# Kernel tuning notes

Measured on AMD Instinct MI355X. Metric: run time of the kernel, lower is better.

## Reference

```python
import jax, jax.numpy as jnp
import numpy as np

N = 100000      # node_size
R = 2000        # rel_size
E = 300000      # triple_size == nnz(adj)
ER = 300000     # nnz of node-to-rel adjacency
EE = 300000     # nnz of node-to-node adjacency
NODE_F = 128
REL_F = 128
ENT_F = NODE_F + REL_F  # 256
DEPTH = 2


def setup_inputs() -> dict:
    key = jax.random.key(0)
    ks = jax.random.split(key, 14)
    return {
        'ent_emb': jax.random.normal(ks[0], (N, NODE_F), jnp.float32) * 0.1,
        'rel_emb': jax.random.normal(ks[1], (R, REL_F), jnp.float32) * 0.1,
        'a_self': jax.random.normal(ks[2], (ENT_F, 1), jnp.float32) * 0.1,
        'a_neigh': jax.random.normal(ks[3], (ENT_F, 1), jnp.float32) * 0.1,
        'a_rel': jax.random.normal(ks[4], (REL_F, 1), jnp.float32) * 0.1,
        'sp_val': jax.random.uniform(ks[5], (E,), jnp.float32),
        'adj_row': jax.random.randint(ks[6], (E,), 0, N),
        'adj_col': jax.random.randint(ks[7], (E,), 0, N),
        'sp_row': jnp.arange(E),
        'sp_col': jax.random.randint(ks[8], (E,), 0, R),
        'rel_row': jax.random.randint(ks[9], (ER,), 0, N),
        'rel_col': jax.random.randint(ks[10], (ER,), 0, R),
        'ent_row': jax.random.randint(ks[11], (EE,), 0, N),
        'ent_col': jax.random.randint(ks[12], (EE,), 0, N),
    }


def _mean_agg(row, col, emb, nrows):
    # tf.sparse_softmax over all-ones values == 1/deg per row -> row mean
    deg = jax.ops.segment_sum(jnp.ones(row.shape, emb.dtype), row, nrows)
    w = 1.0 / deg[row]
    return jax.ops.segment_sum(w[:, None] * emb[col], row, nrows)


def _segment_softmax(vals, seg, nseg):
    m = jax.ops.segment_max(vals, seg, nseg)
    e = jnp.exp(vals - m[seg])
    s = jax.ops.segment_sum(e, seg, nseg)
    return e / s[seg]


def reference(ent_emb, rel_emb, a_self, a_neigh, a_rel, sp_val,
              adj_row, adj_col, sp_row, sp_col, rel_row, rel_col, ent_row, ent_col):
    # initial features: mean-aggregated entity + relation features
    rel_feat = _mean_agg(rel_row, rel_col, rel_emb, N)
    ent_feat = _mean_agg(ent_row, ent_col, ent_emb, N)
    features = jax.nn.relu(jnp.concatenate([ent_feat, rel_feat], axis=-1))  # [N, ENT_F]
    outputs = [features]

    # per-edge relation attention term: (T,R) sparse @ (rel_emb @ a_rel); constant across depth
    rel_proj = (rel_emb @ a_rel)[:, 0]                               # [R]
    rel_attn = jax.ops.segment_sum(sp_val * rel_proj[sp_col], sp_row, E)  # [E]

    att = None
    for _ in range(DEPTH):
        a_s = (features @ a_self)[:, 0]    # [N]
        a_n = (features @ a_neigh)[:, 0]   # [N]
        att = rel_attn + a_s[adj_row] + a_n[adj_col]          # [E]
        att = jax.nn.leaky_relu(att, negative_slope=0.2)
        att = _segment_softmax(att, adj_row, N)               # row-wise sparse softmax
        features = jax.nn.relu(
            jax.ops.segment_sum(att[:, None] * features[adj_col], adj_row, N))
        outputs.append(features)

    out = jnp.concatenate(outputs, axis=-1)  # [N, ENT_F*(DEPTH+1)]
    return out, att
```

## Files before the change

kernel.cpp:

```cpp
#include <hip/hip_runtime.h>

#define NODE_F 128
#define ENT_F  256
#define LDO    768
#define NEG_INF -3.4e38f

typedef float vf4 __attribute__((ext_vector_type(4)));


__global__ void count3_k(const int* __restrict__ r0, const int* __restrict__ r1,
                         const int* __restrict__ r2, int E0, int E1, int E2,
                         int* __restrict__ deg3, int N) {
    int i = blockIdx.x * blockDim.x + threadIdx.x;
    int y = blockIdx.y;
    const int* rp = (y == 0) ? r0 : (y == 1) ? r1 : r2;
    int Eg = (y == 0) ? E0 : (y == 1) ? E1 : E2;
    if (i < Eg) atomicAdd(&deg3[(size_t)y * N + rp[i]], 1);
}

__global__ void alloc3_k(const int* __restrict__ deg3, int* __restrict__ tot3,
                         int* __restrict__ start3, int* __restrict__ cur3, int N) {
    int y = blockIdx.y;
    int i = blockIdx.x * blockDim.x + threadIdx.x;
    int lane = threadIdx.x & 63;
    int d = (i < N) ? deg3[(size_t)y * N + i] : 0;
    int v = d;
    #pragma unroll
    for (int o = 1; o < 64; o <<= 1) {
        int t = __shfl_up(v, o);
        if (lane >= o) v += t;
    }
    int wsum = __shfl(v, 63);
    int base = 0;
    if (lane == 63) base = atomicAdd(&tot3[y], wsum);
    base = __shfl(base, 63);
    if (i < N) {
        int st = base + v - d;
        start3[(size_t)y * N + i] = st;
        cur3[(size_t)y * N + i] = st;
    }
}

__global__ void scatter3_k(const int* __restrict__ r0, const int* __restrict__ c0,
                           const int* __restrict__ r1, const int* __restrict__ c1,
                           const int* __restrict__ r2, const int* __restrict__ c2,
                           int E0, int E1, int E2, int* __restrict__ cur3,
                           int* __restrict__ col_adj, int* __restrict__ eid_adj,
                           int* __restrict__ row_adj,
                           int* __restrict__ col_ent, int* __restrict__ col_rel,
                           const float* __restrict__ sp_val, const int* __restrict__ sp_col,
                           const float* __restrict__ proj, float* __restrict__ rel_attn_s,
                           int N) {
    int e = blockIdx.x * blockDim.x + threadIdx.x;
    int y = blockIdx.y;
    const int* rp = (y == 0) ? r0 : (y == 1) ? r1 : r2;
    const int* cp = (y == 0) ? c0 : (y == 1) ? c1 : c2;
    int* colp = (y == 0) ? col_adj : (y == 1) ? col_ent : col_rel;
    int Eg = (y == 0) ? E0 : (y == 1) ? E1 : E2;
    if (e >= Eg) return;
    int r = rp[e];
    int pos = atomicAdd(&cur3[(size_t)y * N + r], 1);
    colp[pos] = cp[e];
    if (y == 0) {
        eid_adj[pos] = e;
        row_adj[pos] = r;
        rel_attn_s[pos] = sp_val[e] * proj[sp_col[e]];
    }
}

__global__ void rel_proj_k(const float* __restrict__ rel_emb, const float* __restrict__ a_rel,
                           float* __restrict__ proj, int R) {
    int r = blockIdx.x * blockDim.x + threadIdx.x;
    if (r >= R) return;
    float s = 0.0f;
    #pragma unroll 4
    for (int f = 0; f < NODE_F; ++f) s += rel_emb[(size_t)r * NODE_F + f] * a_rel[f];
    proj[r] = s;
}

__global__ void edge_att_k(const int* __restrict__ row_s, const int* __restrict__ col_s,
                           const float* __restrict__ rel_attn_s,
                           const float* __restrict__ a_s, const float* __restrict__ a_n,
                           float* __restrict__ att_raw, int E) {
    int p = blockIdx.x * blockDim.x + threadIdx.x;
    if (p >= E) return;
    float v = rel_attn_s[p] + a_s[row_s[p]] + a_n[col_s[p]];
    att_raw[p] = v >= 0.0f ? v : 0.2f * v;
}


__global__ void meanagg_fused_k(const int* __restrict__ st_ent, const int* __restrict__ dg_ent,
                                const int* __restrict__ col_ent,
                                const int* __restrict__ st_rel, const int* __restrict__ dg_rel,
                                const int* __restrict__ col_rel,
                                const float* __restrict__ ent_emb, const float* __restrict__ rel_emb,
                                const float* __restrict__ a_self, const float* __restrict__ a_neigh,
                                float* __restrict__ out,
                                float* __restrict__ a_s_out, float* __restrict__ a_n_out, int N) {
    int n = blockIdx.x * (blockDim.x >> 6) + (threadIdx.x >> 6);
    int lane = threadIdx.x & 63;
    if (n >= N) return;

    float2 ea = {0.0f, 0.0f};
    {
        int s = st_ent[n], deg = dg_ent[n];
        int p = 0;
        for (; p + 4 <= deg; p += 4) {
            int c0 = col_ent[s + p], c1 = col_ent[s + p + 1];
            int c2 = col_ent[s + p + 2], c3 = col_ent[s + p + 3];
            float2 v0 = reinterpret_cast<const float2*>(&ent_emb[(size_t)c0 * NODE_F])[lane];
            float2 v1 = reinterpret_cast<const float2*>(&ent_emb[(size_t)c1 * NODE_F])[lane];
            float2 v2 = reinterpret_cast<const float2*>(&ent_emb[(size_t)c2 * NODE_F])[lane];
            float2 v3 = reinterpret_cast<const float2*>(&ent_emb[(size_t)c3 * NODE_F])[lane];
            ea.x += v0.x + v1.x + v2.x + v3.x;
            ea.y += v0.y + v1.y + v2.y + v3.y;
        }
        for (; p < deg; ++p) {
            float2 v = reinterpret_cast<const float2*>(&ent_emb[(size_t)col_ent[s + p] * NODE_F])[lane];
            ea.x += v.x; ea.y += v.y;
        }
        if (deg > 0) { float w = 1.0f / (float)deg; ea.x *= w; ea.y *= w; }
    }

    float2 ra = {0.0f, 0.0f};
    {
        int s = st_rel[n], deg = dg_rel[n];
        int p = 0;
        for (; p + 4 <= deg; p += 4) {
            int c0 = col_rel[s + p], c1 = col_rel[s + p + 1];
            int c2 = col_rel[s + p + 2], c3 = col_rel[s + p + 3];
            float2 v0 = reinterpret_cast<const float2*>(&rel_emb[(size_t)c0 * NODE_F])[lane];
            float2 v1 = reinterpret_cast<const float2*>(&rel_emb[(size_t)c1 * NODE_F])[lane];
            float2 v2 = reinterpret_cast<const float2*>(&rel_emb[(size_t)c2 * NODE_F])[lane];
            float2 v3 = reinterpret_cast<const float2*>(&rel_emb[(size_t)c3 * NODE_F])[lane];
            ra.x += v0.x + v1.x + v2.x + v3.x;
            ra.y += v0.y + v1.y + v2.y + v3.y;
        }
        for (; p < deg; ++p) {
            float2 v = reinterpret_cast<const float2*>(&rel_emb[(size_t)col_rel[s + p] * NODE_F])[lane];
            ra.x += v.x; ra.y += v.y;
        }
        if (deg > 0) { float w = 1.0f / (float)deg; ra.x *= w; ra.y *= w; }
    }

    ea.x = ea.x > 0.0f ? ea.x : 0.0f;  ea.y = ea.y > 0.0f ? ea.y : 0.0f;
    ra.x = ra.x > 0.0f ? ra.x : 0.0f;  ra.y = ra.y > 0.0f ? ra.y : 0.0f;

    reinterpret_cast<float2*>(&out[(size_t)n * LDO])[lane] = ea;
    reinterpret_cast<float2*>(&out[(size_t)n * LDO + NODE_F])[lane] = ra;

    float2 se = reinterpret_cast<const float2*>(a_self)[lane];
    float2 sr = reinterpret_cast<const float2*>(a_self)[64 + lane];
    float2 ne = reinterpret_cast<const float2*>(a_neigh)[lane];
    float2 nr = reinterpret_cast<const float2*>(a_neigh)[64 + lane];
    float ds = ea.x * se.x + ea.y * se.y + ra.x * sr.x + ra.y * sr.y;
    float dn = ea.x * ne.x + ea.y * ne.y + ra.x * nr.x + ra.y * nr.y;
    #pragma unroll
    for (int o = 32; o > 0; o >>= 1) {
        ds += __shfl_xor(ds, o);
        dn += __shfl_xor(dn, o);
    }
    if (lane == 0) { a_s_out[n] = ds; a_n_out[n] = dn; }
}

template <int NT>
__global__ void attn_agg_slim_k(const int* __restrict__ st, const int* __restrict__ dg,
                                const int* __restrict__ col_s, const int* __restrict__ eid_s,
                                const float* __restrict__ att_raw,
                                const float* __restrict__ a_self, const float* __restrict__ a_neigh,
                                float* __restrict__ a_s_out, float* __restrict__ a_n_out,
                                float* __restrict__ out, int src, int dst,
                                float* __restrict__ att_out, int N) {
    int n = blockIdx.x * (blockDim.x >> 6) + (threadIdx.x >> 6);
    int lane = threadIdx.x & 63;
    if (n >= N) return;
    int s = st[n];
    int deg = dg[n];
    float4 acc = {0.0f, 0.0f, 0.0f, 0.0f};

    if (deg > 0) {
        if (deg <= 64) {
            float myv = NEG_INF;
            int mycol = 0;
            if (lane < deg) {
                mycol = col_s[s + lane];
                myv = att_raw[s + lane];
            }
            float m = myv;
            #pragma unroll
            for (int o = 32; o > 0; o >>= 1) {
                float x = __shfl_xor(m, o);
                m = x > m ? x : m;
            }
            float ex = (lane < deg) ? __expf(myv - m) : 0.0f;
            float ssum = ex;
            #pragma unroll
            for (int o = 32; o > 0; o >>= 1) ssum += __shfl_xor(ssum, o);
            float myatt = ex / ssum;
            if (att_out && lane < deg) {
                if (NT) __builtin_nontemporal_store(myatt, &att_out[eid_s[s + lane]]);
                else    att_out[eid_s[s + lane]] = myatt;
            }

            int p = 0;
            for (; p + 4 <= deg; p += 4) {
                float a0 = __shfl(myatt, p),     a1 = __shfl(myatt, p + 1);
                float a2 = __shfl(myatt, p + 2), a3 = __shfl(myatt, p + 3);
                int c0 = __shfl(mycol, p),     c1 = __shfl(mycol, p + 1);
                int c2 = __shfl(mycol, p + 2), c3 = __shfl(mycol, p + 3);
                float4 v0 = reinterpret_cast<const float4*>(&out[(size_t)c0 * LDO + src])[lane];
                float4 v1 = reinterpret_cast<const float4*>(&out[(size_t)c1 * LDO + src])[lane];
                float4 v2 = reinterpret_cast<const float4*>(&out[(size_t)c2 * LDO + src])[lane];
                float4 v3 = reinterpret_cast<const float4*>(&out[(size_t)c3 * LDO + src])[lane];
                acc.x += a0 * v0.x + a1 * v1.x + a2 * v2.x + a3 * v3.x;
                acc.y += a0 * v0.y + a1 * v1.y + a2 * v2.y + a3 * v3.y;
                acc.z += a0 * v0.z + a1 * v1.z + a2 * v2.z + a3 * v3.z;
                acc.w += a0 * v0.w + a1 * v1.w + a2 * v2.w + a3 * v3.w;
            }
            for (; p < deg; ++p) {
                float a = __shfl(myatt, p);
                int c = __shfl(mycol, p);
                float4 v = reinterpret_cast<const float4*>(&out[(size_t)c * LDO + src])[lane];
                acc.x += a * v.x; acc.y += a * v.y; acc.z += a * v.z; acc.w += a * v.w;
            }
        } else {
            float m = NEG_INF;
            for (int p = s + lane; p < s + deg; p += 64) {
                float v = att_raw[p];
                m = v > m ? v : m;
            }
            #pragma unroll
            for (int o = 32; o > 0; o >>= 1) {
                float x = __shfl_xor(m, o);
                m = x > m ? x : m;
            }
            float ssum = 0.0f;
            for (int p = s + lane; p < s + deg; p += 64) ssum += __expf(att_raw[p] - m);
            #pragma unroll
            for (int o = 32; o > 0; o >>= 1) ssum += __shfl_xor(ssum, o);
            float inv = 1.0f / ssum;
            for (int p = s; p < s + deg; ++p) {
                int c = col_s[p];
                float a = __expf(att_raw[p] - m) * inv;
                if (att_out && lane == 0) att_out[eid_s[p]] = a;
                float4 fv = reinterpret_cast<const float4*>(&out[(size_t)c * LDO + src])[lane];
                acc.x += a * fv.x; acc.y += a * fv.y; acc.z += a * fv.z; acc.w += a * fv.w;
            }
        }
    }

    acc.x = acc.x > 0.0f ? acc.x : 0.0f;
    acc.y = acc.y > 0.0f ? acc.y : 0.0f;
    acc.z = acc.z > 0.0f ? acc.z : 0.0f;
    acc.w = acc.w > 0.0f ? acc.w : 0.0f;
    float* dstp = &out[(size_t)n * LDO + dst] + (size_t)lane * 4;
    if (NT) {
        vf4 v; v.x = acc.x; v.y = acc.y; v.z = acc.z; v.w = acc.w;
        __builtin_nontemporal_store(v, reinterpret_cast<vf4*>(dstp));
    } else {
        *reinterpret_cast<float4*>(dstp) = acc;
    }

    if (a_s_out) {
        float4 s4 = reinterpret_cast<const float4*>(a_self)[lane];
        float4 n4 = reinterpret_cast<const float4*>(a_neigh)[lane];
        float ds = acc.x * s4.x + acc.y * s4.y + acc.z * s4.z + acc.w * s4.w;
        float dn = acc.x * n4.x + acc.y * n4.y + acc.z * n4.z + acc.w * n4.w;
        #pragma unroll
        for (int o = 32; o > 0; o >>= 1) {
            ds += __shfl_xor(ds, o);
            dn += __shfl_xor(dn, o);
        }
        if (lane == 0) { a_s_out[n] = ds; a_n_out[n] = dn; }
    }
}


extern "C" void kernel_launch(void* const* d_in, const int* in_sizes, int n_in,
                              void* d_out, int out_size, void* d_ws, size_t ws_size,
                              hipStream_t stream) {
    const float* ent_emb = (const float*)d_in[0];
    const float* rel_emb = (const float*)d_in[1];
    const float* a_self  = (const float*)d_in[2];
    const float* a_neigh = (const float*)d_in[3];
    const float* a_rel   = (const float*)d_in[4];
    const float* sp_val  = (const float*)d_in[5];
    const int*   adj_row = (const int*)d_in[6];
    const int*   adj_col = (const int*)d_in[7];
    const int*   sp_col  = (const int*)d_in[9];
    const int*   rel_row = (const int*)d_in[10];
    const int*   rel_col = (const int*)d_in[11];
    const int*   ent_row = (const int*)d_in[12];
    const int*   ent_col = (const int*)d_in[13];

    const int N  = in_sizes[0] / NODE_F;
    const int R  = in_sizes[1] / NODE_F;
    const int E  = in_sizes[5];
    const int ER = in_sizes[10];
    const int EE = in_sizes[12];

    float* out = (float*)d_out;
    float* att_out = out + (size_t)N * LDO;

    const int TB = 256;
    int maxE = E > EE ? E : EE; if (ER > maxE) maxE = ER;

    char* w = (char*)d_ws;
    int* deg3    = (int*)w;  w += (size_t)3 * N * 4;
    int* tot3    = (int*)w;  w += 4 * 4;
    int* start3  = (int*)w;  w += (size_t)3 * N * 4;
    int* cur3    = (int*)w;  w += (size_t)3 * N * 4;
    int* col_adj = (int*)w;  w += (size_t)E * 4;
    int* eid_adj = (int*)w;  w += (size_t)E * 4;
    int* row_adj = (int*)w;  w += (size_t)E * 4;
    int* col_ent = (int*)w;  w += (size_t)EE * 4;
    int* col_rel = (int*)w;  w += (size_t)ER * 4;
    float* rel_attn_s = (float*)w;  w += (size_t)E * 4;
    float* att_raw    = (float*)w;  w += (size_t)E * 4;
    float* proj       = (float*)w;  w += (size_t)R * 4;
    float* a_s0       = (float*)w;  w += (size_t)N * 4;
    float* a_n0       = (float*)w;  w += (size_t)N * 4;
    float* a_s1       = (float*)w;  w += (size_t)N * 4;
    float* a_n1       = (float*)w;  w += (size_t)N * 4;

    int* st_adj = start3;          int* dg_adj = deg3;
    int* st_ent = start3 + N;      int* dg_ent = deg3 + N;
    int* st_rel = start3 + 2 * N;  int* dg_rel = deg3 + 2 * N;

    const int gE = (E + TB - 1) / TB;

    rel_proj_k<<<(R + TB - 1) / TB, TB, 0, stream>>>(rel_emb, a_rel, proj, R);

    hipMemsetAsync(deg3, 0, ((size_t)3 * N + 4) * sizeof(int), stream);
    {
        dim3 g((maxE + TB - 1) / TB, 3);
        count3_k<<<g, TB, 0, stream>>>(adj_row, ent_row, rel_row, E, EE, ER, deg3, N);
    }
    {
        dim3 g((N + TB - 1) / TB, 3);
        alloc3_k<<<g, TB, 0, stream>>>(deg3, tot3, start3, cur3, N);
    }
    {
        dim3 g((maxE + TB - 1) / TB, 3);
        scatter3_k<<<g, TB, 0, stream>>>(adj_row, adj_col, ent_row, ent_col, rel_row, rel_col,
                                         E, EE, ER, cur3, col_adj, eid_adj, row_adj,
                                         col_ent, col_rel, sp_val, sp_col, proj, rel_attn_s, N);
    }

    meanagg_fused_k<<<(N + 3) / 4, 256, 0, stream>>>(st_ent, dg_ent, col_ent,
                                                     st_rel, dg_rel, col_rel,
                                                     ent_emb, rel_emb, a_self, a_neigh,
                                                     out, a_s0, a_n0, N);

    edge_att_k<<<gE, TB, 0, stream>>>(row_adj, col_adj, rel_attn_s, a_s0, a_n0, att_raw, E);
    attn_agg_slim_k<0><<<(N + 3) / 4, 256, 0, stream>>>(st_adj, dg_adj, col_adj, eid_adj,
                                                        att_raw, a_self, a_neigh, a_s1, a_n1,
                                                        out, 0, ENT_F, nullptr, N);

    edge_att_k<<<gE, TB, 0, stream>>>(row_adj, col_adj, rel_attn_s, a_s1, a_n1, att_raw, E);
    attn_agg_slim_k<1><<<(N + 3) / 4, 256, 0, stream>>>(st_adj, dg_adj, col_adj, eid_adj,
                                                        att_raw, nullptr, nullptr, nullptr, nullptr,
                                                        out, ENT_F, 2 * ENT_F, att_out, N);
}
```

Baseline: 378.5 us.

## Replace atomic CSR allocation with ordered three-pass prefix scan; drop gather unrolling

Replaces the wave-level scan plus atomicAdd offset allocation with a deterministic three-kernel prefix scan (block sums, scan of block sums, per-element scan). Row starts become monotonic in node order, so neighbour lists sit contiguously in row order and nearby rows share cache lines. It also removes the 4-way manual unrolling in the mean-aggregation and attention-aggregation gather loops, which lowers register pressure but exposes less memory-level parallelism. The scan adds two extra kernel launches and limits the node count to 512*256 blocks.

```diff
diff --git a/kernel.cpp b/kernel.cpp
--- a/kernel.cpp
+++ b/kernel.cpp
@@ -18,26 +18,53 @@
     if (i < Eg) atomicAdd(&deg3[(size_t)y * N + rp[i]], 1);
 }
 
-__global__ void alloc3_k(const int* __restrict__ deg3, int* __restrict__ tot3,
-                         int* __restrict__ start3, int* __restrict__ cur3, int N) {
+__global__ void blocksum3_k(const int* __restrict__ deg3, int* __restrict__ bs3, int N) {
+    __shared__ int s[256];
     int y = blockIdx.y;
-    int i = blockIdx.x * blockDim.x + threadIdx.x;
-    int lane = threadIdx.x & 63;
-    int d = (i < N) ? deg3[(size_t)y * N + i] : 0;
-    int v = d;
-    #pragma unroll
-    for (int o = 1; o < 64; o <<= 1) {
-        int t = __shfl_up(v, o);
-        if (lane >= o) v += t;
-    }
-    int wsum = __shfl(v, 63);
-    int base = 0;
-    if (lane == 63) base = atomicAdd(&tot3[y], wsum);
-    base = __shfl(base, 63);
+    int i = blockIdx.x * 256 + threadIdx.x;
+    s[threadIdx.x] = (i < N) ? deg3[(size_t)y * N + i] : 0;
+    __syncthreads();
+    for (int o = 128; o > 0; o >>= 1) {
+        if (threadIdx.x < o) s[threadIdx.x] += s[threadIdx.x + o];
+        __syncthreads();
+    }
+    if (threadIdx.x == 0) bs3[y * 512 + blockIdx.x] = s[0];
+}
+
+__global__ void scanbsum3_k(int* __restrict__ bs3, int nb) {
+    __shared__ int s[512];
+    int y = blockIdx.x;
+    int tid = threadIdx.x;
+    int v = (tid < nb) ? bs3[y * 512 + tid] : 0;
+    s[tid] = v;
+    __syncthreads();
+    for (int o = 1; o < 512; o <<= 1) {
+        int t = (tid >= o) ? s[tid - o] : 0;
+        __syncthreads();
+        s[tid] += t;
+        __syncthreads();
+    }
+    if (tid < nb) bs3[y * 512 + tid] = s[tid] - v;
+}
+
+__global__ void scandeg3_k(const int* __restrict__ deg3, const int* __restrict__ bs3,
+                           int* __restrict__ rs3, int* __restrict__ cur3, int N) {
+    __shared__ int s[256];
+    int y = blockIdx.y;
+    int i = blockIdx.x * 256 + threadIdx.x;
+    int v = (i < N) ? deg3[(size_t)y * N + i] : 0;
+    s[threadIdx.x] = v;
+    __syncthreads();
+    for (int o = 1; o < 256; o <<= 1) {
+        int t = (threadIdx.x >= o) ? s[threadIdx.x - o] : 0;
+        __syncthreads();
+        s[threadIdx.x] += t;
+        __syncthreads();
+    }
     if (i < N) {
-        int st = base + v - d;
-        start3[(size_t)y * N + i] = st;
-        cur3[(size_t)y * N + i] = st;
+        int rs = bs3[y * 512 + blockIdx.x] + s[threadIdx.x] - v;
+        rs3[(size_t)y * N + i] = rs;
+        cur3[(size_t)y * N + i] = rs;
     }
 }
 
@@ -104,19 +131,8 @@
     float2 ea = {0.0f, 0.0f};
     {
         int s = st_ent[n], deg = dg_ent[n];
-        int p = 0;
-        for (; p + 4 <= deg; p += 4) {
-            int c0 = col_ent[s + p], c1 = col_ent[s + p + 1];
-            int c2 = col_ent[s + p + 2], c3 = col_ent[s + p + 3];
-            float2 v0 = reinterpret_cast<const float2*>(&ent_emb[(size_t)c0 * NODE_F])[lane];
-            float2 v1 = reinterpret_cast<const float2*>(&ent_emb[(size_t)c1 * NODE_F])[lane];
-            float2 v2 = reinterpret_cast<const float2*>(&ent_emb[(size_t)c2 * NODE_F])[lane];
-            float2 v3 = reinterpret_cast<const float2*>(&ent_emb[(size_t)c3 * NODE_F])[lane];
-            ea.x += v0.x + v1.x + v2.x + v3.x;
-            ea.y += v0.y + v1.y + v2.y + v3.y;
-        }
-        for (; p < deg; ++p) {
-            float2 v = reinterpret_cast<const float2*>(&ent_emb[(size_t)col_ent[s + p] * NODE_F])[lane];
+        for (int p = s; p < s + deg; ++p) {
+            float2 v = reinterpret_cast<const float2*>(&ent_emb[(size_t)col_ent[p] * NODE_F])[lane];
             ea.x += v.x; ea.y += v.y;
         }
         if (deg > 0) { float w = 1.0f / (float)deg; ea.x *= w; ea.y *= w; }
@@ -125,19 +141,8 @@
     float2 ra = {0.0f, 0.0f};
     {
         int s = st_rel[n], deg = dg_rel[n];
-        int p = 0;
-        for (; p + 4 <= deg; p += 4) {
-            int c0 = col_rel[s + p], c1 = col_rel[s + p + 1];
-            int c2 = col_rel[s + p + 2], c3 = col_rel[s + p + 3];
-            float2 v0 = reinterpret_cast<const float2*>(&rel_emb[(size_t)c0 * NODE_F])[lane];
-            float2 v1 = reinterpret_cast<const float2*>(&rel_emb[(size_t)c1 * NODE_F])[lane];
-            float2 v2 = reinterpret_cast<const float2*>(&rel_emb[(size_t)c2 * NODE_F])[lane];
-            float2 v3 = reinterpret_cast<const float2*>(&rel_emb[(size_t)c3 * NODE_F])[lane];
-            ra.x += v0.x + v1.x + v2.x + v3.x;
-            ra.y += v0.y + v1.y + v2.y + v3.y;
-        }
-        for (; p < deg; ++p) {
-            float2 v = reinterpret_cast<const float2*>(&rel_emb[(size_t)col_rel[s + p] * NODE_F])[lane];
+        for (int p = s; p < s + deg; ++p) {
+            float2 v = reinterpret_cast<const float2*>(&rel_emb[(size_t)col_rel[p] * NODE_F])[lane];
             ra.x += v.x; ra.y += v.y;
         }
         if (deg > 0) { float w = 1.0f / (float)deg; ra.x *= w; ra.y *= w; }
@@ -201,23 +206,7 @@
                 if (NT) __builtin_nontemporal_store(myatt, &att_out[eid_s[s + lane]]);
                 else    att_out[eid_s[s + lane]] = myatt;
             }
-
-            int p = 0;
-            for (; p + 4 <= deg; p += 4) {
-                float a0 = __shfl(myatt, p),     a1 = __shfl(myatt, p + 1);
-                float a2 = __shfl(myatt, p + 2), a3 = __shfl(myatt, p + 3);
-                int c0 = __shfl(mycol, p),     c1 = __shfl(mycol, p + 1);
-                int c2 = __shfl(mycol, p + 2), c3 = __shfl(mycol, p + 3);
-                float4 v0 = reinterpret_cast<const float4*>(&out[(size_t)c0 * LDO + src])[lane];
-                float4 v1 = reinterpret_cast<const float4*>(&out[(size_t)c1 * LDO + src])[lane];
-                float4 v2 = reinterpret_cast<const float4*>(&out[(size_t)c2 * LDO + src])[lane];
-                float4 v3 = reinterpret_cast<const float4*>(&out[(size_t)c3 * LDO + src])[lane];
-                acc.x += a0 * v0.x + a1 * v1.x + a2 * v2.x + a3 * v3.x;
-                acc.y += a0 * v0.y + a1 * v1.y + a2 * v2.y + a3 * v3.y;
-                acc.z += a0 * v0.z + a1 * v1.z + a2 * v2.z + a3 * v3.z;
-                acc.w += a0 * v0.w + a1 * v1.w + a2 * v2.w + a3 * v3.w;
-            }
-            for (; p < deg; ++p) {
+            for (int p = 0; p < deg; ++p) {
                 float a = __shfl(myatt, p);
                 int c = __shfl(mycol, p);
                 float4 v = reinterpret_cast<const float4*>(&out[(size_t)c * LDO + src])[lane];
@@ -303,13 +292,14 @@
     float* att_out = out + (size_t)N * LDO;
 
     const int TB = 256;
+    const int nb = (N + 255) / 256;
     int maxE = E > EE ? E : EE; if (ER > maxE) maxE = ER;
 
     char* w = (char*)d_ws;
     int* deg3    = (int*)w;  w += (size_t)3 * N * 4;
-    int* tot3    = (int*)w;  w += 4 * 4;
-    int* start3  = (int*)w;  w += (size_t)3 * N * 4;
+    int* rs3     = (int*)w;  w += (size_t)3 * N * 4;
     int* cur3    = (int*)w;  w += (size_t)3 * N * 4;
+    int* bs3     = (int*)w;  w += (size_t)3 * 512 * 4;
     int* col_adj = (int*)w;  w += (size_t)E * 4;
     int* eid_adj = (int*)w;  w += (size_t)E * 4;
     int* row_adj = (int*)w;  w += (size_t)E * 4;
@@ -323,22 +313,24 @@
     float* a_s1       = (float*)w;  w += (size_t)N * 4;
     float* a_n1       = (float*)w;  w += (size_t)N * 4;
 
-    int* st_adj = start3;          int* dg_adj = deg3;
-    int* st_ent = start3 + N;      int* dg_ent = deg3 + N;
-    int* st_rel = start3 + 2 * N;  int* dg_rel = deg3 + 2 * N;
+    int* st_adj = rs3;          int* dg_adj = deg3;
+    int* st_ent = rs3 + N;      int* dg_ent = deg3 + N;
+    int* st_rel = rs3 + 2 * N;  int* dg_rel = deg3 + 2 * N;
 
     const int gE = (E + TB - 1) / TB;
 
     rel_proj_k<<<(R + TB - 1) / TB, TB, 0, stream>>>(rel_emb, a_rel, proj, R);
 
-    hipMemsetAsync(deg3, 0, ((size_t)3 * N + 4) * sizeof(int), stream);
+    hipMemsetAsync(deg3, 0, (size_t)3 * N * sizeof(int), stream);
     {
         dim3 g((maxE + TB - 1) / TB, 3);
         count3_k<<<g, TB, 0, stream>>>(adj_row, ent_row, rel_row, E, EE, ER, deg3, N);
     }
     {
-        dim3 g((N + TB - 1) / TB, 3);
-        alloc3_k<<<g, TB, 0, stream>>>(deg3, tot3, start3, cur3, N);
+        dim3 g(nb, 3);
+        blocksum3_k<<<g, 256, 0, stream>>>(deg3, bs3, N);
+        scanbsum3_k<<<3, 512, 0, stream>>>(bs3, nb);
+        scandeg3_k<<<g, 256, 0, stream>>>(deg3, bs3, rs3, cur3, N);
     }
     {
         dim3 g((maxE + TB - 1) / TB, 3);
```

New measurement: 345.5 us. 8.7% less time.
